# Kernel tuning notes

Hardware: AMD Instinct MI355X
Metric: run time of the kernel (lower is better)

Reference implementation:

```python
import jax, jax.numpy as jnp
import numpy as np

K = 3
KK = K * K


def _conv1x1(x, w, b):
    # x: [B,Ci,H,W], w: [Co,Ci]
    return jnp.einsum('bihw,oi->bohw', x, w) + b[None, :, None, None]


def _conv3x3(x, w, b):
    y = jax.lax.conv_general_dilated(x, w, (1, 1), ((1, 1), (1, 1)),
                                     dimension_numbers=('NCHW', 'OIHW', 'NCHW'))
    return y + b[None, :, None, None]


def _deform_conv3x3(x, offset, w, b):
    # Deformable conv v1, kernel 3x3, stride 1, pad 1, dilation 1, 1 deformable group.
    # x: [B,C,H,W]; offset: [B,2*KK,H,W] (dy,dx interleaved per kernel tap); w: [Co,C,3,3]
    B, C, H, W = x.shape
    dt = x.dtype
    off = offset.reshape(B, KK, 2, H, W)
    ky, kx = jnp.meshgrid(jnp.arange(K, dtype=dt), jnp.arange(K, dtype=dt), indexing='ij')
    ky = ky.reshape(KK)
    kx = kx.reshape(KK)
    # sampling locations: out_pos - pad + kernel_tap + learned offset
    base_y = jnp.arange(H, dtype=dt) - 1.0  # pad = 1
    base_x = jnp.arange(W, dtype=dt) - 1.0
    sy = base_y[None, None, :, None] + ky[None, :, None, None] + off[:, :, 0]  # [B,KK,H,W]
    sx = base_x[None, None, None, :] + kx[None, :, None, None] + off[:, :, 1]
    y0 = jnp.floor(sy)
    x0 = jnp.floor(sx)
    ty = sy - y0
    tx = sx - x0

    def gather(iy, ix):
        valid = ((iy >= 0) & (iy <= H - 1) & (ix >= 0) & (ix <= W - 1)).astype(dt)
        iyc = jnp.clip(iy, 0, H - 1).astype(jnp.int32)
        ixc = jnp.clip(ix, 0, W - 1).astype(jnp.int32)
        vals = jax.vmap(lambda img, a, c: img[:, a, c])(x, iyc, ixc)  # [B,C,KK,H,W]
        return vals * valid[:, None]

    w00 = ((1 - ty) * (1 - tx))[:, None]
    w01 = ((1 - ty) * tx)[:, None]
    w10 = (ty * (1 - tx))[:, None]
    w11 = (ty * tx)[:, None]
    sampled = (gather(y0, x0) * w00 + gather(y0, x0 + 1) * w01 +
               gather(y0 + 1, x0) * w10 + gather(y0 + 1, x0 + 1) * w11)  # [B,C,KK,H,W]
    Co = w.shape[0]
    out = jnp.einsum('bikhw,oik->bohw', sampled, w.reshape(Co, C, KK))
    return out + b[None, :, None, None]


def _branch(features, dw, db, ow, ob, tw, tb):
    h = _conv1x1(features, dw, db)
    off = _conv3x3(h, ow, ob)  # offset-predicting conv inside DFConv2d
    return jax.nn.relu(_deform_conv3x3(h, off, tw, tb))


def setup_inputs() -> dict:
    key = jax.random.key(0)
    ks = jax.random.split(key, 13)
    C = 256
    s1 = 1.0 / np.sqrt(C)          # kaiming_normal a=1 for 1x1 conv
    s3 = 1.0 / np.sqrt(C * KK)     # 3x3 conv
    so = 0.01                       # small offset-conv weights -> modest offsets
    f = lambda k, s, sc: jax.random.normal(k, s, dtype=jnp.float32) * sc
    return {
        'features': f(ks[0], (4, C, 64, 64), 1.0),
        'agg_down_w': f(ks[1], (C, C), s1),
        'agg_down_b': jnp.zeros((C,), jnp.float32),
        'agg_off_w': f(ks[2], (2 * KK, C, K, K), so),
        'agg_off_b': jnp.zeros((2 * KK,), jnp.float32),
        'agg_w': f(ks[3], (C, C, K, K), s3),
        'agg_b': jnp.zeros((C,), jnp.float32),
        'appr_down_w': f(ks[4], (C, C), s1),
        'appr_down_b': jnp.zeros((C,), jnp.float32),
        'appr_off_w': f(ks[5], (2 * KK, C, K, K), so),
        'appr_off_b': jnp.zeros((2 * KK,), jnp.float32),
        'appr_w': f(ks[6], (C, C, K, K), s3),
        'appr_b': jnp.zeros((C,), jnp.float32),
    }


def reference(features, agg_down_w, agg_down_b, agg_off_w, agg_off_b, agg_w, agg_b,
              appr_down_w, appr_down_b, appr_off_w, appr_off_b, appr_w, appr_b):
    agg = _branch(features, agg_down_w, agg_down_b, agg_off_w, agg_off_b, agg_w, agg_b)
    appr = _branch(features, appr_down_w, appr_down_b, appr_off_w, appr_off_b, appr_w, appr_b)
    return (agg, appr)
```

## Files before the change

### kernel.cpp

```cpp
#include <hip/hip_runtime.h>

#define HWP 4096
#define NPIX 4194304
#define KDIM 2304

typedef __attribute__((ext_vector_type(4))) float f32x4;
typedef __attribute__((ext_vector_type(4))) int   i32x4;
typedef __attribute__((ext_vector_type(8))) short short8;
typedef __attribute__((ext_vector_type(4))) unsigned short bf16x4;
typedef __attribute__((ext_vector_type(4))) unsigned short u16x4;

__device__ __forceinline__ unsigned short bf16_rne(float f) {
    unsigned int u = __builtin_bit_cast(unsigned int, f);
    u += 0x7FFFu + ((u >> 16) & 1u);
    return (unsigned short)(u >> 16);
}

__device__ __forceinline__ float bf2f(unsigned short u) {
    return __builtin_bit_cast(float, (unsigned int)u << 16);
}

__device__ __forceinline__ float u2f_lo(unsigned int u) {
    return __builtin_bit_cast(float, u << 16);
}

__device__ __forceinline__ float u2f_hi(unsigned int u) {
    return __builtin_bit_cast(float, u & 0xFFFF0000u);
}

__device__ __forceinline__ unsigned int cvt_pk_bf16(float lo, float hi) {
    unsigned int r;
    asm("v_cvt_pk_bf16_f32 %0, %1, %2" : "=v"(r) : "v"(lo), "v"(hi));
    return r;
}

__device__ __forceinline__ void gload_lds16(const void* g, void* l) {
    __builtin_amdgcn_global_load_lds((const __attribute__((address_space(1))) void*)g,
                                     (__attribute__((address_space(3))) void*)l, 16, 0, 0);
}

__global__ void prep_all_kernel(const float* __restrict__ x, unsigned short* __restrict__ fbt,
                                const float* __restrict__ dw0, const float* __restrict__ dw1,
                                const float* __restrict__ tw0, const float* __restrict__ tw1,
                                const float* __restrict__ ow0, const float* __restrict__ ow1,
                                unsigned short* __restrict__ w1b2,
                                unsigned short* __restrict__ w2A,
                                unsigned short* __restrict__ w2o) {
    __shared__ float T[64][65];
    int b = blockIdx.x;
    int t = threadIdx.x;
    if (b < 1024) {
        int pt = b & 63, ct = (b >> 6) & 3, bb = b >> 8;
        int lane = t & 63;
        int r = t >> 6;
        int c0 = ct * 64, p0 = pt * 64;
        const float* xb = x + (size_t)(bb * 256 + c0) * HWP + p0;
#pragma unroll
        for (int rr = 0; rr < 16; ++rr) {
            int ci = r * 16 + rr;
            T[ci][lane] = xb[(size_t)ci * HWP + lane];
        }
        __syncthreads();
        unsigned short* ob = fbt + ((size_t)bb * HWP + p0) * 256 + c0;
#pragma unroll
        for (int rr = 0; rr < 16; ++rr) {
            int px = r * 16 + rr;
            ob[(size_t)px * 256 + lane] = bf16_rne(T[lane][px]);
        }
        return;
    }
    int idx = (b - 1024) * 256 + t;
    if (idx < 131072) {
        int br = idx >> 16;
        int i  = idx & 65535;
        const float* dw = br ? dw1 : dw0;
        w1b2[idx] = bf16_rne(dw[i]);
    } else if (idx < 131072 + 1179648) {
        int j = idx - 131072;
        int br = j >= 589824;
        int i  = br ? j - 589824 : j;
        const float* tw = br ? tw1 : tw0;
        int cg = i / 147456;
        int r  = i - cg * 147456;
        int tap = r >> 14;
        int r2 = r & 16383;
        int s  = r2 >> 11;
        int fr = (r2 >> 9) & 3;
        int l  = (r2 >> 3) & 63;
        int e  = r2 & 7;
        int o  = cg * 64 + fr * 16 + (l & 15);
        int ci = s * 32 + ((l >> 4) << 3) + e;
        w2A[j] = bf16_rne(tw[(o * 256 + ci) * 9 + tap]);
    } else {
        int j = idx - 131072 - 1179648;
        int br = j >= 73728;
        int i  = br ? j - 73728 : j;
        const float* ow = br ? ow1 : ow0;
        int m = i / 2304;
        int k = i - m * 2304;
        int tap = k >> 8;
        int ci  = k & 255;
        w2o[j] = (m < 18) ? bf16_rne(ow[(m * 256 + ci) * 9 + tap]) : (unsigned short)0;
    }
}

__global__ void prep_w2_kernel(const float* __restrict__ tw0, const float* __restrict__ tw1,
                               unsigned short* __restrict__ w2) {
    int idx = blockIdx.x * 256 + threadIdx.x;
    int br = idx >= 589824;
    int i  = br ? idx - 589824 : idx;
    const float* tw = br ? tw1 : tw0;
    int ci = i & 255;
    int r  = i >> 8;
    int tap = r % 9;
    int o   = r / 9;
    w2[idx] = bf16_rne(tw[(o * 256 + ci) * 9 + tap]);
}

__global__ void prep_ow2_kernel(const float* __restrict__ ow0, const float* __restrict__ ow1,
                                float* __restrict__ owt) {
    int idx = blockIdx.x * 256 + threadIdx.x;
    int br = idx >= 41472;
    int i  = br ? idx - 41472 : idx;
    const float* ow = br ? ow1 : ow0;
    int co = i % 18;
    int r  = i / 18;
    int k  = r % 9;
    int ci = r / 9;
    owt[idx] = ow[(co * 256 + ci) * 9 + k];
}

__global__ void prep_w12_kernel(const float* __restrict__ dw0, const float* __restrict__ dw1,
                                unsigned short* __restrict__ w1b) {
    int idx = blockIdx.x * 256 + threadIdx.x;
    int br = idx >> 16;
    int i  = idx & 65535;
    const float* dw = br ? dw1 : dw0;
    w1b[idx] = bf16_rne(dw[i]);
}

__global__ void prep_fb16_kernel(const float* __restrict__ x, unsigned short* __restrict__ fbt) {
    __shared__ float T[64][65];
    int pt = blockIdx.x;
    int ct = blockIdx.y;
    int bb = blockIdx.z;
    int t = threadIdx.x;
    int lane = t & 63;
    int r = t >> 6;
    int c0 = ct * 64, p0 = pt * 64;
    const float* xb = x + (size_t)(bb * 256 + c0) * HWP + p0;
#pragma unroll
    for (int rr = 0; rr < 16; ++rr) {
        int ci = r * 16 + rr;
        T[ci][lane] = xb[(size_t)ci * HWP + lane];
    }
    __syncthreads();
    unsigned short* ob = fbt + ((size_t)bb * HWP + p0) * 256 + c0;
#pragma unroll
    for (int rr = 0; rr < 16; ++rr) {
        int px = r * 16 + rr;
        ob[(size_t)px * 256 + lane] = bf16_rne(T[lane][px]);
    }
}

__launch_bounds__(256)
__global__ void gemm1x1_kernel(const unsigned short* __restrict__ w1b2,
                               const unsigned short* __restrict__ fbt,
                               const float* __restrict__ db0, const float* __restrict__ db1,
                               float* __restrict__ h2, unsigned short* __restrict__ ht2,
                               int write_h) {
    __shared__ unsigned short As[128 * 64];
    __shared__ unsigned short Bs[64 * 64];
    int pt = blockIdx.x;
    int ot = blockIdx.y;
    int z  = blockIdx.z;
    int bb = z & 3;
    int br = z >> 2;
    const unsigned short* w1b = w1b2 + (size_t)br * 65536;
    const float* db = br ? db1 : db0;
    int t  = threadIdx.x;
    int l  = t & 63;
    int w  = t >> 6;
    int wr = w >> 1, wc = w & 1;
    int o0 = ot * 128, p0 = pt * 64;
    const unsigned short* fb = fbt + (size_t)bb * HWP * 256;
    f32x4 acc[4][2];
#pragma unroll
    for (int i = 0; i < 4; ++i)
#pragma unroll
        for (int j = 0; j < 2; ++j) acc[i][j] = (f32x4){0.f, 0.f, 0.f, 0.f};

    for (int ks = 0; ks < 4; ++ks) {
        int k0 = ks * 64;
#pragma unroll
        for (int rA = 0; rA < 4; ++rA) {
            int s = rA * 256 + t;
            int row = s >> 3, cg = (s & 7) ^ (row & 7);
            gload_lds16(w1b + (size_t)(o0 + row) * 256 + k0 + cg * 8, As + s * 8);
        }
#pragma unroll
        for (int rB = 0; rB < 2; ++rB) {
            int s = rB * 256 + t;
            int row = s >> 3, cg = (s & 7) ^ (row & 7);
            gload_lds16(fb + (size_t)(p0 + row) * 256 + k0 + cg * 8, Bs + s * 8);
        }
        __syncthreads();
#pragma unroll
        for (int half = 0; half < 2; ++half) {
            short8 a[4], b[2];
#pragma unroll
            for (int fr = 0; fr < 4; ++fr) {
                int row = wr * 64 + fr * 16 + (l & 15);
                int oct = half * 4 + (l >> 4);
                a[fr] = *reinterpret_cast<const short8*>(As + row * 64 + ((oct ^ (row & 7)) * 8));
            }
#pragma unroll
            for (int fc = 0; fc < 2; ++fc) {
                int row = wc * 32 + fc * 16 + (l & 15);
                int oct = half * 4 + (l >> 4);
                b[fc] = *reinterpret_cast<const short8*>(Bs + row * 64 + ((oct ^ (row & 7)) * 8));
            }
#pragma unroll
            for (int fr = 0; fr < 4; ++fr)
#pragma unroll
                for (int fc = 0; fc < 2; ++fc)
                    acc[fr][fc] = __builtin_amdgcn_mfma_f32_16x16x32_bf16(a[fr], b[fc], acc[fr][fc], 0, 0, 0);
        }
        __syncthreads();
    }

    float* hb = h2 + (size_t)br * NPIX + (size_t)bb * 256 * HWP;
    unsigned short* htb = ht2 + (size_t)br * NPIX + (size_t)bb * HWP * 256;
#pragma unroll
    for (int fr = 0; fr < 4; ++fr) {
        int o = o0 + wr * 64 + fr * 16 + ((l >> 4) << 2);
#pragma unroll
        for (int fc = 0; fc < 2; ++fc) {
            int p = p0 + wc * 32 + fc * 16 + (l & 15);
            f32x4 v;
#pragma unroll
            for (int reg = 0; reg < 4; ++reg) {
                v[reg] = acc[fr][fc][reg] + db[o + reg];
                if (write_h) hb[(size_t)(o + reg) * HWP + p] = v[reg];
            }
            uint2 pk;
            pk.x = cvt_pk_bf16(v[0], v[1]);
            pk.y = cvt_pk_bf16(v[2], v[3]);
            *reinterpret_cast<uint2*>(htb + (size_t)p * 256 + o) = pk;
        }
    }
}

__launch_bounds__(256)
__global__ void off_mfma_kernel(const unsigned short* __restrict__ w2o,
                                const unsigned short* __restrict__ ht2,
                                const float* __restrict__ ob0, const float* __restrict__ ob1,
                                float* __restrict__ dwq, unsigned short* __restrict__ dcq) {
    __shared__ float red[4][1152];
    int id = blockIdx.x;
    int br = id >> 8;
    int bb = (id >> 6) & 3;
    int y  = id & 63;
    const unsigned short* wA = w2o + (size_t)br * 73728;
    const unsigned short* htb = ht2 + (size_t)br * NPIX + (size_t)bb * HWP * 256;
    const float* ob = br ? ob1 : ob0;
    int t = threadIdx.x;
    int l = t & 63;
    int w = t >> 6;
    short8 zero = {};
    f32x4 acc[2][4];
#pragma unroll
    for (int i = 0; i < 2; ++i)
#pragma unroll
        for (int j = 0; j < 4; ++j) acc[i][j] = (f32x4){0.f, 0.f, 0.f, 0.f};

    for (int tap = 0; tap < 9; ++tap) {
        int ky = tap / 3, kx = tap % 3;
        int yy = y + ky - 1;
        bool vy = (yy >= 0) && (yy < 64);
        int cyy = min(max(yy, 0), 63);
#pragma unroll
        for (int sh = 0; sh < 2; ++sh) {
            int s = w * 2 + sh;
            short8 a[2], b[4];
#pragma unroll
            for (int fr = 0; fr < 2; ++fr)
                a[fr] = *reinterpret_cast<const short8*>(
                    wA + (size_t)(fr * 16 + (l & 15)) * KDIM + tap * 256 + s * 32 + ((l >> 4) << 3));
#pragma unroll
            for (int fc = 0; fc < 4; ++fc) {
                int px = fc * 16 + (l & 15);
                int xx = px + kx - 1;
                bool v = vy && (xx >= 0) && (xx < 64);
                int cxx = min(max(xx, 0), 63);
                short8 bv = *reinterpret_cast<const short8*>(
                    htb + (size_t)(cyy * 64 + cxx) * 256 + s * 32 + ((l >> 4) << 3));
                b[fc] = v ? bv : zero;
            }
#pragma unroll
            for (int fr = 0; fr < 2; ++fr)
#pragma unroll
                for (int fc = 0; fc < 4; ++fc)
                    acc[fr][fc] = __builtin_amdgcn_mfma_f32_16x16x32_bf16(a[fr], b[fc], acc[fr][fc], 0, 0, 0);
        }
    }

#pragma unroll
    for (int fr = 0; fr < 2; ++fr)
#pragma unroll
        for (int fc = 0; fc < 4; ++fc) {
            int px = fc * 16 + (l & 15);
#pragma unroll
            for (int reg = 0; reg < 4; ++reg) {
                int co = fr * 16 + ((l >> 4) << 2) + reg;
                if (co < 18) red[w][co * 64 + px] = acc[fr][fc][reg];
            }
        }
    __syncthreads();

    size_t dbase = ((size_t)(br * 4 + bb) * 9) * 4096 + (size_t)(y * 64);
    for (int e = t; e < 576; e += 256) {
        int tap = e >> 6, px = e & 63;
        int c0 = 2 * tap, c1 = 2 * tap + 1;
        float dy = ob[c0] + red[0][c0 * 64 + px] + red[1][c0 * 64 + px]
                          + red[2][c0 * 64 + px] + red[3][c0 * 64 + px];
        float dx = ob[c1] + red[0][c1 * 64 + px] + red[1][c1 * 64 + px]
                          + red[2][c1 * 64 + px] + red[3][c1 * 64 + px];
        int ky = tap / 3, kx = tap % 3;
        float sy = (float)(y - 1 + ky) + dy;
        float sx = (float)(px - 1 + kx) + dx;
        float y0f = floorf(sy), x0f = floorf(sx);
        float ty = sy - y0f, tx = sx - x0f;
        int iy0 = (int)y0f, ix0 = (int)x0f;
        int iy1 = iy0 + 1, ix1 = ix0 + 1;
        bool vy0 = (iy0 >= 0) & (iy0 < 64);
        bool vy1 = (iy1 >= 0) & (iy1 < 64);
        bool vx0 = (ix0 >= 0) & (ix0 < 64);
        bool vx1 = (ix1 >= 0) & (ix1 < 64);
        int cy0 = min(max(iy0, 0), 63), cy1 = min(max(iy1, 0), 63);
        int cx0 = min(max(ix0, 0), 63), cx1 = min(max(ix1, 0), 63);
        f32x4 ww;
        ww[0] = (1.f - ty) * (1.f - tx) * ((vy0 & vx0) ? 1.f : 0.f);
        ww[1] = (1.f - ty) * tx * ((vy0 & vx1) ? 1.f : 0.f);
        ww[2] = ty * (1.f - tx) * ((vy1 & vx0) ? 1.f : 0.f);
        ww[3] = ty * tx * ((vy1 & vx1) ? 1.f : 0.f);
        u16x4 pc;
        pc[0] = (unsigned short)(cy0 * 64 + cx0);
        pc[1] = (unsigned short)(cy0 * 64 + cx1);
        pc[2] = (unsigned short)(cy1 * 64 + cx0);
        pc[3] = (unsigned short)(cy1 * 64 + cx1);
        size_t di = dbase + (size_t)tap * 4096 + px;
        *reinterpret_cast<f32x4*>(dwq + di * 4) = ww;
        *reinterpret_cast<u16x4*>(dcq + di * 4) = pc;
    }
}

__global__ void off_conv_part_kernel(const float* __restrict__ h2, const float* __restrict__ owt2,
                                     float* __restrict__ part2) {
    int y  = blockIdx.x & 63;
    int bb = blockIdx.x >> 6;
    int c  = blockIdx.y;
    int br = blockIdx.z;
    const float* h = h2 + (size_t)br * NPIX;
    const float* owt = owt2 + (size_t)br * 41472;
    float* part = part2 + (size_t)br * 2359296;
    int t  = threadIdx.x;
    int x  = t & 63;
    int wv = __builtin_amdgcn_readfirstlane(t >> 6);
    int  toff[9];
    bool tval[9];
#pragma unroll
    for (int ky = 0; ky < 3; ++ky) {
        int yy = y + ky - 1;
        bool vy = (yy >= 0) && (yy < 64);
        int cyy = min(max(yy, 0), 63);
#pragma unroll
        for (int kx = 0; kx < 3; ++kx) {
            int xx = x + kx - 1;
            tval[ky * 3 + kx] = vy && (xx >= 0) && (xx < 64);
            toff[ky * 3 + kx] = cyy * 64 + min(max(xx, 0), 63);
        }
    }
    float acc[18];
#pragma unroll
    for (int co = 0; co < 18; ++co) acc[co] = 0.f;
    int ci0 = c * 32 + wv * 8;
    const float* hb = h + (size_t)(bb * 256 + ci0) * HWP;
#pragma unroll
    for (int i = 0; i < 8; ++i) {
        const float* hc = hb + i * HWP;
        const float* wci = owt + (size_t)(ci0 + i) * 162;
#pragma unroll
        for (int k = 0; k < 9; ++k) {
            float hv = hc[toff[k]];
            hv = tval[k] ? hv : 0.f;
            const float* wk = wci + k * 18;
#pragma unroll
            for (int co = 0; co < 18; ++co)
                acc[co] = fmaf(wk[co], hv, acc[co]);
        }
    }
    __shared__ float red[4][18][64];
    int wvl = t >> 6;
#pragma unroll
    for (int co = 0; co < 18; ++co) red[wvl][co][x] = acc[co];
    __syncthreads();
    if (wvl == 0) {
#pragma unroll
        for (int co = 0; co < 18; ++co) {
            float s = red[0][co][x] + red[1][co][x] + red[2][co][x] + red[3][co][x];
            part[(size_t)c * 294912 + ((bb * 18 + co) << 12) + (y << 6) + x] = s;
        }
    }
}

__global__ void off_reduce2_kernel(const float* __restrict__ part2,
                                   const float* __restrict__ ob0, const float* __restrict__ ob1,
                                   float* __restrict__ off2) {
    int idx = blockIdx.x * 256 + threadIdx.x;
    int br = idx >= 294912;
    int i  = br ? idx - 294912 : idx;
    const float* part = part2 + (size_t)br * 2359296;
    const float* b = br ? ob1 : ob0;
    int co = (i >> 12) % 18;
    float s = b[co];
#pragma unroll
    for (int c = 0; c < 8; ++c) s += part[(size_t)c * 294912 + i];
    off2[idx] = s;
}

__launch_bounds__(256, 2)
__global__ void dgemm_fused_kernel(const unsigned short* __restrict__ w2b,
                                   const unsigned short* __restrict__ ht2,
                                   const float* __restrict__ dwq,
                                   const unsigned short* __restrict__ dcq,
                                   const float* __restrict__ tb0,
                                   const float* __restrict__ tb1,
                                   float* __restrict__ out) {
    __shared__ unsigned short Bs[2][64 * 256];
    int id = blockIdx.x;
    int sw = (id & 7) * 64 + (id >> 3);
    int br = sw >> 8;
    int mt = sw & 255;
    int bb = mt >> 6;
    int y  = mt & 63;
    const unsigned short* w2f = w2b + (size_t)br * 589824;
    const unsigned short* htb = ht2 + (size_t)br * NPIX + (size_t)bb * HWP * 256;
    const float* bias = br ? tb1 : tb0;
    size_t dbase = ((size_t)(br * 4 + bb) * 9) * 4096 + (size_t)(y * 64);
    int t = threadIdx.x;
    int l = t & 63;
    int w = t >> 6;
    int wvu = __builtin_amdgcn_readfirstlane(w);
    int le = l << 2;

    f32x4 acc[4][4];
#pragma unroll
    for (int i = 0; i < 4; ++i)
#pragma unroll
        for (int j = 0; j < 4; ++j) acc[i][j] = (f32x4){0.f, 0.f, 0.f, 0.f};

#define STAGE_B(TAPV, WB)                                                          \
    do {                                                                           \
        const float* dwt = dwq + (dbase + (size_t)(TAPV) * 4096) * 4;              \
        const unsigned short* dct = dcq + (dbase + (size_t)(TAPV) * 4096) * 4;     \
        _Pragma("unroll")                                                          \
        for (int i_ = 0; i_ < 16; ++i_) {                                          \
            int px = wvu * 16 + i_;                                                \
            f32x4 ww = *reinterpret_cast<const f32x4*>(dwt + (size_t)px * 4);      \
            u16x4 pc = *reinterpret_cast<const u16x4*>(dct + (size_t)px * 4);      \
            int b00 = ((int)pc[0] << 8) + le;                                      \
            int b01 = ((int)pc[1] << 8) + le;                                      \
            int b10 = ((int)pc[2] << 8) + le;                                      \
            int b11 = ((int)pc[3] << 8) + le;                                      \
            uint2 u00 = *reinterpret_cast<const uint2*>(htb + b00);                \
            uint2 u01 = *reinterpret_cast<const uint2*>(htb + b01);                \
            uint2 u10 = *reinterpret_cast<const uint2*>(htb + b10);                \
            uint2 u11 = *reinterpret_cast<const uint2*>(htb + b11);                \
            float s0 = fmaf(ww[0], u2f_lo(u00.x),                                  \
                       fmaf(ww[1], u2f_lo(u01.x),                                  \
                       fmaf(ww[2], u2f_lo(u10.x), ww[3] * u2f_lo(u11.x))));        \
            float s1 = fmaf(ww[0], u2f_hi(u00.x),                                  \
                       fmaf(ww[1], u2f_hi(u01.x),                                  \
                       fmaf(ww[2], u2f_hi(u10.x), ww[3] * u2f_hi(u11.x))));        \
            float s2 = fmaf(ww[0], u2f_lo(u00.y),                                  \
                       fmaf(ww[1], u2f_lo(u01.y),                                  \
                       fmaf(ww[2], u2f_lo(u10.y), ww[3] * u2f_lo(u11.y))));        \
            float s3 = fmaf(ww[0], u2f_hi(u00.y),                                  \
                       fmaf(ww[1], u2f_hi(u01.y),                                  \
                       fmaf(ww[2], u2f_hi(u10.y), ww[3] * u2f_hi(u11.y))));        \
            uint2 pk;                                                              \
            pk.x = cvt_pk_bf16(s0, s1);                                            \
            pk.y = cvt_pk_bf16(s2, s3);                                            \
            int g = l >> 1, sub = l & 1;                                           \
            *reinterpret_cast<uint2*>((WB) + px * 256 +                            \
                (((g ^ (px & 7)) << 3) | (sub << 2))) = pk;                        \
        }                                                                          \
    } while (0)

#define COMPUTE_TAP(TAPV, RB)                                                      \
    do {                                                                           \
        const unsigned short* wtapf = w2f + (size_t)(wvu * 9 + (TAPV)) * 16384;    \
        short8 aA[4], aB[4];                                                       \
        _Pragma("unroll")                                                          \
        for (int fr = 0; fr < 4; ++fr)                                             \
            aA[fr] = *reinterpret_cast<const short8*>(wtapf + fr * 512 + (l << 3));\
        _Pragma("unroll")                                                          \
        for (int fr = 0; fr < 4; ++fr)                                             \
            aB[fr] = *reinterpret_cast<const short8*>(wtapf + (4 + fr) * 512 + (l << 3)); \
        _Pragma("unroll")                                                          \
        for (int s = 0; s < 8; ++s) {                                              \
            short8 aC[4];                                                          \
            if (s < 6) {                                                           \
                _Pragma("unroll")                                                  \
                for (int fr = 0; fr < 4; ++fr)                                     \
                    aC[fr] = *reinterpret_cast<const short8*>(                     \
                        wtapf + (size_t)((s + 2) * 4 + fr) * 512 + (l << 3));      \
            }                                                                      \
            short8 b[4];                                                           \
            _Pragma("unroll")                                                      \
            for (int fc = 0; fc < 4; ++fc) {                                       \
                int prow = fc * 16 + (l & 15);                                     \
                int cg8 = (s << 2) + (l >> 4);                                     \
                b[fc] = *reinterpret_cast<const short8*>(                          \
                    (RB) + prow * 256 + ((cg8 ^ (prow & 7)) << 3));                \
            }                                                                      \
            __builtin_amdgcn_s_setprio(1);                                         \
            _Pragma("unroll")                                                      \
            for (int fr = 0; fr < 4; ++fr)                                         \
                _Pragma("unroll")                                                  \
                for (int fc = 0; fc < 4; ++fc)                                     \
                    acc[fr][fc] = __builtin_amdgcn_mfma_f32_16x16x32_bf16(         \
                        aA[fr], b[fc], acc[fr][fc], 0, 0, 0);                      \
            __builtin_amdgcn_s_setprio(0);                                         \
            if (s < 7) {                                                           \
                _Pragma("unroll")                                                  \
                for (int fr = 0; fr < 4; ++fr) { aA[fr] = aB[fr]; aB[fr] = aC[fr]; } \
            }                                                                      \
        }                                                                          \
    } while (0)

    STAGE_B(0, Bs[0]);
    __syncthreads();
#pragma unroll 1
    for (int it = 0; it < 4; ++it) {
        int tap = it * 2;
        COMPUTE_TAP(tap, Bs[0]);
        STAGE_B(tap + 1, Bs[1]);
        __syncthreads();
        COMPUTE_TAP(tap + 1, Bs[1]);
        STAGE_B(tap + 2, Bs[0]);
        __syncthreads();
    }
    COMPUTE_TAP(8, Bs[0]);
#undef STAGE_B
#undef COMPUTE_TAP

    float* outp = out + (size_t)br * NPIX + (size_t)(bb * 256) * HWP + y * 64;
#pragma unroll
    for (int fr = 0; fr < 4; ++fr) {
        int o = wvu * 64 + fr * 16 + ((l >> 4) << 2);
#pragma unroll
        for (int fc = 0; fc < 4; ++fc) {
            int pxc = fc * 16 + (l & 15);
#pragma unroll
            for (int reg = 0; reg < 4; ++reg) {
                float v = acc[fr][fc][reg] + bias[o + reg];
                outp[(size_t)(o + reg) * HWP + pxc] = fmaxf(v, 0.f);
            }
        }
    }
}

__launch_bounds__(256)
__global__ void sample2_kernel(const unsigned short* __restrict__ ht, const float* __restrict__ off,
                               unsigned short* __restrict__ sm, int b0) {
    int y   = blockIdx.x;
    int tap = blockIdx.y;
    int bb  = b0 + blockIdx.z;
    int t   = threadIdx.x;
    int lane = t & 63;
    int wv  = t >> 6;
    int ky = tap / 3, kx = tap % 3;
    const unsigned short* htb = ht + (size_t)bb * HWP * 256;
    const float* offy = off + ((bb * 18 + 2 * tap) * 64 + y) * 64;
    const float* offx = off + ((bb * 18 + 2 * tap + 1) * 64 + y) * 64;
    int mrow = ((bb - b0) * 64 + y) * 64;
#pragma unroll 4
    for (int i = 0; i < 16; ++i) {
        int px = wv * 16 + i;
        float dy = offy[px];
        float dx = offx[px];
        float sy = (float)(y - 1 + ky) + dy;
        float sx = (float)(px - 1 + kx) + dx;
        float y0f = floorf(sy), x0f = floorf(sx);
        float ty = sy - y0f, tx = sx - x0f;
        int iy0 = (int)y0f, ix0 = (int)x0f;
        int iy1 = iy0 + 1, ix1 = ix0 + 1;
        bool vy0 = (iy0 >= 0) & (iy0 < 64);
        bool vy1 = (iy1 >= 0) & (iy1 < 64);
        bool vx0 = (ix0 >= 0) & (ix0 < 64);
        bool vx1 = (ix1 >= 0) & (ix1 < 64);
        int cy0 = min(max(iy0, 0), 63), cy1 = min(max(iy1, 0), 63);
        int cx0 = min(max(ix0, 0), 63), cx1 = min(max(ix1, 0), 63);
        float w00 = (1.f - ty) * (1.f - tx) * ((vy0 & vx0) ? 1.f : 0.f);
        float w01 = (1.f - ty) * tx * ((vy0 & vx1) ? 1.f : 0.f);
        float w10 = ty * (1.f - tx) * ((vy1 & vx0) ? 1.f : 0.f);
        float w11 = ty * tx * ((vy1 & vx1) ? 1.f : 0.f);
        int le = lane << 2;
        bf16x4 q00 = *reinterpret_cast<const bf16x4*>(htb + ((cy0 * 64 + cx0) << 8) + le);
        bf16x4 q01 = *reinterpret_cast<const bf16x4*>(htb + ((cy0 * 64 + cx1) << 8) + le);
        bf16x4 q10 = *reinterpret_cast<const bf16x4*>(htb + ((cy1 * 64 + cx0) << 8) + le);
        bf16x4 q11 = *reinterpret_cast<const bf16x4*>(htb + ((cy1 * 64 + cx1) << 8) + le);
        f32x4 s;
#pragma unroll
        for (int j = 0; j < 4; ++j)
            s[j] = fmaf(w00, bf2f(q00[j]),
                   fmaf(w01, bf2f(q01[j]),
                   fmaf(w10, bf2f(q10[j]), w11 * bf2f(q11[j]))));
        uint2 pk;
        pk.x = cvt_pk_bf16(s[0], s[1]);
        pk.y = cvt_pk_bf16(s[2], s[3]);
        *reinterpret_cast<uint2*>(sm + (size_t)(mrow + px) * KDIM + tap * 256 + lane * 4) = pk;
    }
}

__launch_bounds__(256)
__global__ void gemm2_kernel(const unsigned short* __restrict__ w2b,
                             const unsigned short* __restrict__ smb, size_t smstride,
                             const float* __restrict__ tb0, const float* __restrict__ tb1,
                             float* __restrict__ out, int mbase) {
    __shared__ unsigned short As[128 * 64];
    __shared__ unsigned short Bs[64 * 64];
    int mt = blockIdx.x;
    int ot = blockIdx.y;
    int br = blockIdx.z;
    const unsigned short* w2 = w2b + (size_t)br * 589824;
    const unsigned short* sm = smb + (size_t)br * smstride;
    const float* bias = br ? tb1 : tb0;
    float* outp = out + (size_t)br * NPIX;
    int t  = threadIdx.x;
    int l  = t & 63;
    int w  = t >> 6;
    int wr = w >> 1, wc = w & 1;
    int o0 = ot * 128, m0 = mt * 64;
    f32x4 acc[4][2];
#pragma unroll
    for (int i = 0; i < 4; ++i)
#pragma unroll
        for (int j = 0; j < 2; ++j) acc[i][j] = (f32x4){0.f, 0.f, 0.f, 0.f};

    for (int ks = 0; ks < KDIM / 64; ++ks) {
        int k0 = ks * 64;
#pragma unroll
        for (int rA = 0; rA < 4; ++rA) {
            int s = rA * 256 + t;
            int row = s >> 3, cg = (s & 7) ^ (row & 7);
            gload_lds16(w2 + (size_t)(o0 + row) * KDIM + k0 + cg * 8, As + s * 8);
        }
#pragma unroll
        for (int rB = 0; rB < 2; ++rB) {
            int s = rB * 256 + t;
            int row = s >> 3, cg = (s & 7) ^ (row & 7);
            gload_lds16(sm + (size_t)(m0 + row) * KDIM + k0 + cg * 8, Bs + s * 8);
        }
        __syncthreads();
#pragma unroll
        for (int half = 0; half < 2; ++half) {
            short8 a[4], b[2];
#pragma unroll
            for (int fr = 0; fr < 4; ++fr) {
                int row = wr * 64 + fr * 16 + (l & 15);
                int oct = half * 4 + (l >> 4);
                a[fr] = *reinterpret_cast<const short8*>(As + row * 64 + ((oct ^ (row & 7)) * 8));
            }
#pragma unroll
            for (int fc = 0; fc < 2; ++fc) {
                int row = wc * 32 + fc * 16 + (l & 15);
                int oct = half * 4 + (l >> 4);
                b[fc] = *reinterpret_cast<const short8*>(Bs + row * 64 + ((oct ^ (row & 7)) * 8));
            }
#pragma unroll
            for (int fr = 0; fr < 4; ++fr)
#pragma unroll
                for (int fc = 0; fc < 2; ++fc)
                    acc[fr][fc] = __builtin_amdgcn_mfma_f32_16x16x32_bf16(a[fr], b[fc], acc[fr][fc], 0, 0, 0);
        }
        __syncthreads();
    }

#pragma unroll
    for (int fr = 0; fr < 4; ++fr) {
        int o = o0 + wr * 64 + fr * 16 + ((l >> 4) << 2);
#pragma unroll
        for (int fc = 0; fc < 2; ++fc) {
            int mg = mbase + m0 + wc * 32 + fc * 16 + (l & 15);
            int bbv = mg >> 12;
            int pix = mg & 4095;
            float* op = outp + (size_t)(bbv * 256) * HWP + pix;
#pragma unroll
            for (int reg = 0; reg < 4; ++reg) {
                float v = acc[fr][fc][reg] + bias[o + reg];
                op[(size_t)(o + reg) * HWP] = fmaxf(v, 0.f);
            }
        }
    }
}

extern "C" void kernel_launch(void* const* d_in, const int* in_sizes, int n_in,
                              void* d_out, int out_size, void* d_ws, size_t ws_size,
                              hipStream_t stream) {
    const float* feat = (const float*)d_in[0];
    char* base = (char*)d_ws;
    float* outp = (float*)d_out;
    const size_t perb = (size_t)HWP * KDIM * 2;

    const float* dw0 = (const float*)d_in[1];
    const float* db0 = (const float*)d_in[2];
    const float* ow0 = (const float*)d_in[3];
    const float* ob0 = (const float*)d_in[4];
    const float* tw0 = (const float*)d_in[5];
    const float* tb0 = (const float*)d_in[6];
    const float* dw1 = (const float*)d_in[7];
    const float* db1 = (const float*)d_in[8];
    const float* ow1 = (const float*)d_in[9];
    const float* ob1 = (const float*)d_in[10];
    const float* tw1 = (const float*)d_in[11];
    const float* tb1 = (const float*)d_in[12];

    bool tierA = ws_size >= 47218688;

    if (tierA) {
        unsigned short* ht2 = (unsigned short*)base;
        unsigned short* w2A = (unsigned short*)(base + 35913728);
        unsigned short* w2o = (unsigned short*)(base + 38273024);
        unsigned short* fbt = (unsigned short*)(base + 38567936);
        unsigned short* w1b2 = (unsigned short*)(base + 46956544);
        float* dwq = (float*)(base + 38567936);
        unsigned short* dcq = (unsigned short*)(base + 38567936 + 4718592);

        hipLaunchKernelGGL(prep_all_kernel, dim3(6720), dim3(256), 0, stream,
                           feat, fbt, dw0, dw1, tw0, tw1, ow0, ow1, w1b2, w2A, w2o);
        hipLaunchKernelGGL(gemm1x1_kernel, dim3(64, 2, 8), dim3(256), 0, stream,
                           w1b2, fbt, db0, db1, (float*)nullptr, ht2, 0);
        hipLaunchKernelGGL(off_mfma_kernel, dim3(512), dim3(256), 0, stream,
                           w2o, ht2, ob0, ob1, dwq, dcq);
        hipLaunchKernelGGL(dgemm_fused_kernel, dim3(512), dim3(256), 0, stream,
                           w2A, ht2, dwq, dcq, tb0, tb1, outp);
        return;
    }

    float* h   = (float*)base;
    float* off = h + NPIX;
    unsigned short* w2 = (unsigned short*)(base + 17956864);
    float* owt = (float*)(base + 19136512);
    unsigned short* ht = (unsigned short*)(base + 19302400);
    unsigned short* smN = (unsigned short*)(base + 27691008);
    float* partN = (float*)(base + 27691008);
    unsigned short* fbtN = (unsigned short*)(base + 27691008 + 9437184);
    unsigned short* w1bN = (unsigned short*)(base + 27691008 + 17825792);

    int nb = 0;
    if (27691008 + 4 * perb <= ws_size) nb = 4;
    else if (27691008 + 2 * perb <= ws_size) nb = 2;
    else nb = 1;

    for (int br = 0; br < 2; ++br) {
        const float* dw = (const float*)d_in[1 + 6 * br];
        const float* db = (const float*)d_in[2 + 6 * br];
        const float* ow = (const float*)d_in[3 + 6 * br];
        const float* ob = (const float*)d_in[4 + 6 * br];
        const float* tw = (const float*)d_in[5 + 6 * br];
        const float* tb = (const float*)d_in[6 + 6 * br];

        hipLaunchKernelGGL(prep_fb16_kernel, dim3(64, 4, 4), dim3(256), 0, stream, feat, fbtN);
        hipLaunchKernelGGL(prep_w12_kernel, dim3(256), dim3(256), 0, stream, dw, dw, w1bN);
        hipLaunchKernelGGL(gemm1x1_kernel, dim3(64, 2, 4), dim3(256), 0, stream,
                           w1bN, fbtN, db, db, h, ht, 1);
        hipLaunchKernelGGL(prep_ow2_kernel, dim3(162), dim3(256), 0, stream, ow, ow, owt);
        hipLaunchKernelGGL(off_conv_part_kernel, dim3(256, 8, 1), dim3(256), 0, stream,
                           h, owt, partN);
        hipLaunchKernelGGL(off_reduce2_kernel, dim3(1152), dim3(256), 0, stream,
                           partN, ob, ob, off);
        hipLaunchKernelGGL(prep_w2_kernel, dim3(2304), dim3(256), 0, stream, tw, tw, w2);

        for (int b0 = 0; b0 < 4; b0 += nb) {
            hipLaunchKernelGGL(sample2_kernel, dim3(64, 9, nb), dim3(256), 0, stream,
                               ht, off, smN, b0);
            hipLaunchKernelGGL(gemm2_kernel, dim3(nb * 64, 2, 1), dim3(256), 0, stream,
                               w2, smN, (size_t)0, tb, tb, outp + br * NPIX, b0 * HWP);
        }
    }
}
```

Measured before the change: 122.1 us.

## Interleave deformable sampling gather with MFMA compute inside each tap

The bilinear gather and LDS staging for the next tap is now split into per-pixel pieces, two per k-step, and interleaved with the MFMA loop of the current tap instead of running as a separate phase. The aim is to hide global-load latency of the gather behind matrix math. The A-fragment register rotation becomes a 3-slot ring buffer indexed by step, and the loop runs per tap with a computed buffer parity. This may raise register pressure and can disturb the instruction schedule.

Result: no change. 122.4 us (+0.3%).

```diff
diff --git a/kernel.cpp b/kernel.cpp
--- a/kernel.cpp
+++ b/kernel.cpp
@@ -460,62 +460,61 @@
 #pragma unroll
         for (int j = 0; j < 4; ++j) acc[i][j] = (f32x4){0.f, 0.f, 0.f, 0.f};
 
-#define STAGE_B(TAPV, WB)                                                          \
+#define STAGE_PX(PX, WB)                                                           \
     do {                                                                           \
-        const float* dwt = dwq + (dbase + (size_t)(TAPV) * 4096) * 4;              \
-        const unsigned short* dct = dcq + (dbase + (size_t)(TAPV) * 4096) * 4;     \
-        _Pragma("unroll")                                                          \
-        for (int i_ = 0; i_ < 16; ++i_) {                                          \
-            int px = wvu * 16 + i_;                                                \
-            f32x4 ww = *reinterpret_cast<const f32x4*>(dwt + (size_t)px * 4);      \
-            u16x4 pc = *reinterpret_cast<const u16x4*>(dct + (size_t)px * 4);      \
-            int b00 = ((int)pc[0] << 8) + le;                                      \
-            int b01 = ((int)pc[1] << 8) + le;                                      \
-            int b10 = ((int)pc[2] << 8) + le;                                      \
-            int b11 = ((int)pc[3] << 8) + le;                                      \
-            uint2 u00 = *reinterpret_cast<const uint2*>(htb + b00);                \
-            uint2 u01 = *reinterpret_cast<const uint2*>(htb + b01);                \
-            uint2 u10 = *reinterpret_cast<const uint2*>(htb + b10);                \
-            uint2 u11 = *reinterpret_cast<const uint2*>(htb + b11);                \
-            float s0 = fmaf(ww[0], u2f_lo(u00.x),                                  \
-                       fmaf(ww[1], u2f_lo(u01.x),                                  \
-                       fmaf(ww[2], u2f_lo(u10.x), ww[3] * u2f_lo(u11.x))));        \
-            float s1 = fmaf(ww[0], u2f_hi(u00.x),                                  \
-                       fmaf(ww[1], u2f_hi(u01.x),                                  \
-                       fmaf(ww[2], u2f_hi(u10.x), ww[3] * u2f_hi(u11.x))));        \
-            float s2 = fmaf(ww[0], u2f_lo(u00.y),                                  \
-                       fmaf(ww[1], u2f_lo(u01.y),                                  \
-                       fmaf(ww[2], u2f_lo(u10.y), ww[3] * u2f_lo(u11.y))));        \
-            float s3 = fmaf(ww[0], u2f_hi(u00.y),                                  \
-                       fmaf(ww[1], u2f_hi(u01.y),                                  \
-                       fmaf(ww[2], u2f_hi(u10.y), ww[3] * u2f_hi(u11.y))));        \
-            uint2 pk;                                                              \
-            pk.x = cvt_pk_bf16(s0, s1);                                            \
-            pk.y = cvt_pk_bf16(s2, s3);                                            \
-            int g = l >> 1, sub = l & 1;                                           \
-            *reinterpret_cast<uint2*>((WB) + px * 256 +                            \
-                (((g ^ (px & 7)) << 3) | (sub << 2))) = pk;                        \
-        }                                                                          \
+        int px_ = (PX);                                                            \
+        f32x4 ww = *reinterpret_cast<const f32x4*>(dwt + (size_t)px_ * 4);         \
+        u16x4 pc = *reinterpret_cast<const u16x4*>(dct + (size_t)px_ * 4);         \
+        int b00 = ((int)pc[0] << 8) + le;                                          \
+        int b01 = ((int)pc[1] << 8) + le;                                          \
+        int b10 = ((int)pc[2] << 8) + le;                                          \
+        int b11 = ((int)pc[3] << 8) + le;                                          \
+        uint2 u00 = *reinterpret_cast<const uint2*>(htb + b00);                    \
+        uint2 u01 = *reinterpret_cast<const uint2*>(htb + b01);                    \
+        uint2 u10 = *reinterpret_cast<const uint2*>(htb + b10);                    \
+        uint2 u11 = *reinterpret_cast<const uint2*>(htb + b11);                    \
+        float s0 = fmaf(ww[0], u2f_lo(u00.x),                                      \
+                   fmaf(ww[1], u2f_lo(u01.x),                                      \
+                   fmaf(ww[2], u2f_lo(u10.x), ww[3] * u2f_lo(u11.x))));            \
+        float s1 = fmaf(ww[0], u2f_hi(u00.x),                                      \
+                   fmaf(ww[1], u2f_hi(u01.x),                                      \
+                   fmaf(ww[2], u2f_hi(u10.x), ww[3] * u2f_hi(u11.x))));            \
+        float s2 = fmaf(ww[0], u2f_lo(u00.y),                                      \
+                   fmaf(ww[1], u2f_lo(u01.y),                                      \
+                   fmaf(ww[2], u2f_lo(u10.y), ww[3] * u2f_lo(u11.y))));            \
+        float s3 = fmaf(ww[0], u2f_hi(u00.y),                                      \
+                   fmaf(ww[1], u2f_hi(u01.y),                                      \
+                   fmaf(ww[2], u2f_hi(u10.y), ww[3] * u2f_hi(u11.y))));            \
+        uint2 pk;                                                                  \
+        pk.x = cvt_pk_bf16(s0, s1);                                                \
+        pk.y = cvt_pk_bf16(s2, s3);                                                \
+        int g = l >> 1, sub = l & 1;                                               \
+        *reinterpret_cast<uint2*>((WB) + px_ * 256 +                               \
+            (((g ^ (px_ & 7)) << 3) | (sub << 2))) = pk;                           \
     } while (0)
 
-#define COMPUTE_TAP(TAPV, RB)                                                      \
+#define TAP_BODY(TAPV, RB, WB, DO_STAGE)                                           \
     do {                                                                           \
         const unsigned short* wtapf = w2f + (size_t)(wvu * 9 + (TAPV)) * 16384;    \
-        short8 aA[4], aB[4];                                                       \
+        const float* dwt = dwq + (dbase + (size_t)((TAPV) + 1) * 4096) * 4;        \
+        const unsigned short* dct = dcq + (dbase + (size_t)((TAPV) + 1) * 4096) * 4; \
+        short8 areg[3][4];                                                         \
         _Pragma("unroll")                                                          \
-        for (int fr = 0; fr < 4; ++fr)                                             \
-            aA[fr] = *reinterpret_cast<const short8*>(wtapf + fr * 512 + (l << 3));\
-        _Pragma("unroll")                                                          \
-        for (int fr = 0; fr < 4; ++fr)                                             \
-            aB[fr] = *reinterpret_cast<const short8*>(wtapf + (4 + fr) * 512 + (l << 3)); \
+        for (int fr = 0; fr < 4; ++fr) {                                           \
+            areg[0][fr] = *reinterpret_cast<const short8*>(wtapf + fr * 512 + (l << 3)); \
+            areg[1][fr] = *reinterpret_cast<const short8*>(wtapf + (4 + fr) * 512 + (l << 3)); \
+        }                                                                          \
         _Pragma("unroll")                                                          \
         for (int s = 0; s < 8; ++s) {                                              \
-            short8 aC[4];                                                          \
             if (s < 6) {                                                           \
                 _Pragma("unroll")                                                  \
                 for (int fr = 0; fr < 4; ++fr)                                     \
-                    aC[fr] = *reinterpret_cast<const short8*>(                     \
+                    areg[(s + 2) % 3][fr] = *reinterpret_cast<const short8*>(      \
                         wtapf + (size_t)((s + 2) * 4 + fr) * 512 + (l << 3));      \
+            }                                                                      \
+            if (DO_STAGE) {                                                        \
+                STAGE_PX(wvu * 16 + s * 2 + 0, WB);                                \
+                STAGE_PX(wvu * 16 + s * 2 + 1, WB);                                \
             }                                                                      \
             short8 b[4];                                                           \
             _Pragma("unroll")                                                      \
@@ -531,30 +530,30 @@
                 _Pragma("unroll")                                                  \
                 for (int fc = 0; fc < 4; ++fc)                                     \
                     acc[fr][fc] = __builtin_amdgcn_mfma_f32_16x16x32_bf16(         \
-                        aA[fr], b[fc], acc[fr][fc], 0, 0, 0);                      \
+                        areg[s % 3][fr], b[fc], acc[fr][fc], 0, 0, 0);             \
             __builtin_amdgcn_s_setprio(0);                                         \
-            if (s < 7) {                                                           \
-                _Pragma("unroll")                                                  \
-                for (int fr = 0; fr < 4; ++fr) { aA[fr] = aB[fr]; aB[fr] = aC[fr]; } \
-            }                                                                      \
         }                                                                          \
     } while (0)
 
-    STAGE_B(0, Bs[0]);
+    {
+        const float* dwt = dwq + (dbase + (size_t)0 * 4096) * 4;
+        const unsigned short* dct = dcq + (dbase + (size_t)0 * 4096) * 4;
+#pragma unroll
+        for (int i_ = 0; i_ < 16; ++i_) {
+            STAGE_PX(wvu * 16 + i_, Bs[0]);
+        }
+    }
     __syncthreads();
 #pragma unroll 1
-    for (int it = 0; it < 4; ++it) {
-        int tap = it * 2;
-        COMPUTE_TAP(tap, Bs[0]);
-        STAGE_B(tap + 1, Bs[1]);
+    for (int tap = 0; tap < 8; ++tap) {
+        unsigned short* rb = Bs[tap & 1];
+        unsigned short* wb = Bs[(tap + 1) & 1];
+        TAP_BODY(tap, rb, wb, 1);
         __syncthreads();
-        COMPUTE_TAP(tap + 1, Bs[1]);
-        STAGE_B(tap + 2, Bs[0]);
-        __syncthreads();
-    }
-    COMPUTE_TAP(8, Bs[0]);
-#undef STAGE_B
-#undef COMPUTE_TAP
+    }
+    TAP_BODY(8, Bs[0], Bs[1], 0);
+#undef TAP_BODY
+#undef STAGE_PX
 
     float* outp = out + (size_t)br * NPIX + (size_t)(bb * 256) * HWP + y * 64;
 #pragma unroll
```

## Warp-specialize deformable GEMM into producer gather and consumer MFMA waves

Applied to the files above, without the earlier changes.

Doubles the block to 512 threads and splits the waves by role: four waves gather and bilinearly interpolate the next tap's samples into LDS while the other four run MFMA on the current tap, synchronising once per tap instead of alternating stage and compute in the same waves. The producer batches its weight and index loads before the gathers, and the consumer rotates three A-fragment register buffers by index instead of copying them. This aims to overlap gather latency with matrix math, at the cost of higher per-block resource use that may reduce occupancy and leaves half the waves idle in each phase.

Measured after the change: 124.3 us. No clear change (+1.8%).

```diff
diff --git a/kernel.cpp b/kernel.cpp
--- a/kernel.cpp
+++ b/kernel.cpp
@@ -429,7 +429,7 @@
     off2[idx] = s;
 }
 
-__launch_bounds__(256, 2)
+__launch_bounds__(512, 2)
 __global__ void dgemm_fused_kernel(const unsigned short* __restrict__ w2b,
                                    const unsigned short* __restrict__ ht2,
                                    const float* __restrict__ dwq,
@@ -452,6 +452,8 @@
     int l = t & 63;
     int w = t >> 6;
     int wvu = __builtin_amdgcn_readfirstlane(w);
+    int pw  = wvu & 3;
+    bool isCons = (wvu < 4);
     int le = l << 2;
 
     f32x4 acc[4][4];
@@ -460,61 +462,65 @@
 #pragma unroll
         for (int j = 0; j < 4; ++j) acc[i][j] = (f32x4){0.f, 0.f, 0.f, 0.f};
 
-#define STAGE_B(TAPV, WB)                                                          \
+#define STAGE_TAP(TAPV, WB)                                                        \
     do {                                                                           \
         const float* dwt = dwq + (dbase + (size_t)(TAPV) * 4096) * 4;              \
         const unsigned short* dct = dcq + (dbase + (size_t)(TAPV) * 4096) * 4;     \
+        f32x4 dwv[16];                                                             \
+        u16x4 dcv[16];                                                             \
         _Pragma("unroll")                                                          \
         for (int i_ = 0; i_ < 16; ++i_) {                                          \
-            int px = wvu * 16 + i_;                                                \
-            f32x4 ww = *reinterpret_cast<const f32x4*>(dwt + (size_t)px * 4);      \
-            u16x4 pc = *reinterpret_cast<const u16x4*>(dct + (size_t)px * 4);      \
-            int b00 = ((int)pc[0] << 8) + le;                                      \
-            int b01 = ((int)pc[1] << 8) + le;                                      \
-            int b10 = ((int)pc[2] << 8) + le;                                      \
-            int b11 = ((int)pc[3] << 8) + le;                                      \
+            int px_ = pw * 16 + i_;                                                \
+            dwv[i_] = *reinterpret_cast<const f32x4*>(dwt + (size_t)px_ * 4);      \
+            dcv[i_] = *reinterpret_cast<const u16x4*>(dct + (size_t)px_ * 4);      \
+        }                                                                          \
+        _Pragma("unroll")                                                          \
+        for (int i_ = 0; i_ < 16; ++i_) {                                          \
+            int px_ = pw * 16 + i_;                                                \
+            int b00 = ((int)dcv[i_][0] << 8) + le;                                 \
+            int b01 = ((int)dcv[i_][1] << 8) + le;                                 \
+            int b10 = ((int)dcv[i_][2] << 8) + le;                                 \
+            int b11 = ((int)dcv[i_][3] << 8) + le;                                 \
             uint2 u00 = *reinterpret_cast<const uint2*>(htb + b00);                \
             uint2 u01 = *reinterpret_cast<const uint2*>(htb + b01);                \
             uint2 u10 = *reinterpret_cast<const uint2*>(htb + b10);                \
             uint2 u11 = *reinterpret_cast<const uint2*>(htb + b11);                \
-            float s0 = fmaf(ww[0], u2f_lo(u00.x),                                  \
-                       fmaf(ww[1], u2f_lo(u01.x),                                  \
-                       fmaf(ww[2], u2f_lo(u10.x), ww[3] * u2f_lo(u11.x))));        \
-            float s1 = fmaf(ww[0], u2f_hi(u00.x),                                  \
-                       fmaf(ww[1], u2f_hi(u01.x),                                  \
-                       fmaf(ww[2], u2f_hi(u10.x), ww[3] * u2f_hi(u11.x))));        \
-            float s2 = fmaf(ww[0], u2f_lo(u00.y),                                  \
-                       fmaf(ww[1], u2f_lo(u01.y),                                  \
-                       fmaf(ww[2], u2f_lo(u10.y), ww[3] * u2f_lo(u11.y))));        \
-            float s3 = fmaf(ww[0], u2f_hi(u00.y),                                  \
-                       fmaf(ww[1], u2f_hi(u01.y),                                  \
-                       fmaf(ww[2], u2f_hi(u10.y), ww[3] * u2f_hi(u11.y))));        \
+            float s0 = fmaf(dwv[i_][0], u2f_lo(u00.x),                             \
+                       fmaf(dwv[i_][1], u2f_lo(u01.x),                             \
+                       fmaf(dwv[i_][2], u2f_lo(u10.x), dwv[i_][3] * u2f_lo(u11.x)))); \
+            float s1 = fmaf(dwv[i_][0], u2f_hi(u00.x),                             \
+                       fmaf(dwv[i_][1], u2f_hi(u01.x),                             \
+                       fmaf(dwv[i_][2], u2f_hi(u10.x), dwv[i_][3] * u2f_hi(u11.x)))); \
+            float s2 = fmaf(dwv[i_][0], u2f_lo(u00.y),                             \
+                       fmaf(dwv[i_][1], u2f_lo(u01.y),                             \
+                       fmaf(dwv[i_][2], u2f_lo(u10.y), dwv[i_][3] * u2f_lo(u11.y)))); \
+            float s3 = fmaf(dwv[i_][0], u2f_hi(u00.y),                             \
+                       fmaf(dwv[i_][1], u2f_hi(u01.y),                             \
+                       fmaf(dwv[i_][2], u2f_hi(u10.y), dwv[i_][3] * u2f_hi(u11.y)))); \
             uint2 pk;                                                              \
             pk.x = cvt_pk_bf16(s0, s1);                                            \
             pk.y = cvt_pk_bf16(s2, s3);                                            \
             int g = l >> 1, sub = l & 1;                                           \
-            *reinterpret_cast<uint2*>((WB) + px * 256 +                            \
-                (((g ^ (px & 7)) << 3) | (sub << 2))) = pk;                        \
+            *reinterpret_cast<uint2*>((WB) + px_ * 256 +                           \
+                (((g ^ (px_ & 7)) << 3) | (sub << 2))) = pk;                       \
         }                                                                          \
     } while (0)
 
 #define COMPUTE_TAP(TAPV, RB)                                                      \
     do {                                                                           \
-        const unsigned short* wtapf = w2f + (size_t)(wvu * 9 + (TAPV)) * 16384;    \
-        short8 aA[4], aB[4];                                                       \
+        const unsigned short* wtapf = w2f + (size_t)(pw * 9 + (TAPV)) * 16384;     \
+        short8 areg[3][4];                                                         \
         _Pragma("unroll")                                                          \
-        for (int fr = 0; fr < 4; ++fr)                                             \
-            aA[fr] = *reinterpret_cast<const short8*>(wtapf + fr * 512 + (l << 3));\
-        _Pragma("unroll")                                                          \
-        for (int fr = 0; fr < 4; ++fr)                                             \
-            aB[fr] = *reinterpret_cast<const short8*>(wtapf + (4 + fr) * 512 + (l << 3)); \
+        for (int fr = 0; fr < 4; ++fr) {                                           \
+            areg[0][fr] = *reinterpret_cast<const short8*>(wtapf + fr * 512 + (l << 3)); \
+            areg[1][fr] = *reinterpret_cast<const short8*>(wtapf + (4 + fr) * 512 + (l << 3)); \
+        }                                                                          \
         _Pragma("unroll")                                                          \
         for (int s = 0; s < 8; ++s) {                                              \
-            short8 aC[4];                                                          \
             if (s < 6) {                                                           \
                 _Pragma("unroll")                                                  \
                 for (int fr = 0; fr < 4; ++fr)                                     \
-                    aC[fr] = *reinterpret_cast<const short8*>(                     \
+                    areg[(s + 2) % 3][fr] = *reinterpret_cast<const short8*>(      \
                         wtapf + (size_t)((s + 2) * 4 + fr) * 512 + (l << 3));      \
             }                                                                      \
             short8 b[4];                                                           \
@@ -531,45 +537,41 @@
                 _Pragma("unroll")                                                  \
                 for (int fc = 0; fc < 4; ++fc)                                     \
                     acc[fr][fc] = __builtin_amdgcn_mfma_f32_16x16x32_bf16(         \
-                        aA[fr], b[fc], acc[fr][fc], 0, 0, 0);                      \
+                        areg[s % 3][fr], b[fc], acc[fr][fc], 0, 0, 0);             \
             __builtin_amdgcn_s_setprio(0);                                         \
-            if (s < 7) {                                                           \
-                _Pragma("unroll")                                                  \
-                for (int fr = 0; fr < 4; ++fr) { aA[fr] = aB[fr]; aB[fr] = aC[fr]; } \
-            }                                                                      \
         }                                                                          \
     } while (0)
 
-    STAGE_B(0, Bs[0]);
+    if (!isCons) STAGE_TAP(0, Bs[0]);
     __syncthreads();
 #pragma unroll 1
-    for (int it = 0; it < 4; ++it) {
-        int tap = it * 2;
-        COMPUTE_TAP(tap, Bs[0]);
-        STAGE_B(tap + 1, Bs[1]);
+    for (int tap = 0; tap < 8; ++tap) {
+        if (isCons) {
+            COMPUTE_TAP(tap, Bs[tap & 1]);
+        } else {
+            STAGE_TAP(tap + 1, Bs[(tap + 1) & 1]);
+        }
         __syncthreads();
-        COMPUTE_TAP(tap + 1, Bs[1]);
-        STAGE_B(tap + 2, Bs[0]);
-        __syncthreads();
-    }
-    COMPUTE_TAP(8, Bs[0]);
-#undef STAGE_B
+    }
+    if (isCons) {
+        COMPUTE_TAP(8, Bs[0]);
+        float* outp = out + (size_t)br * NPIX + (size_t)(bb * 256) * HWP + y * 64;
+#pragma unroll
+        for (int fr = 0; fr < 4; ++fr) {
+            int o = pw * 64 + fr * 16 + ((l >> 4) << 2);
+#pragma unroll
+            for (int fc = 0; fc < 4; ++fc) {
+                int pxc = fc * 16 + (l & 15);
+#pragma unroll
+                for (int reg = 0; reg < 4; ++reg) {
+                    float v = acc[fr][fc][reg] + bias[o + reg];
+                    outp[(size_t)(o + reg) * HWP + pxc] = fmaxf(v, 0.f);
+                }
+            }
+        }
+    }
+#undef STAGE_TAP
 #undef COMPUTE_TAP
-
-    float* outp = out + (size_t)br * NPIX + (size_t)(bb * 256) * HWP + y * 64;
-#pragma unroll
-    for (int fr = 0; fr < 4; ++fr) {
-        int o = wvu * 64 + fr * 16 + ((l >> 4) << 2);
-#pragma unroll
-        for (int fc = 0; fc < 4; ++fc) {
-            int pxc = fc * 16 + (l & 15);
-#pragma unroll
-            for (int reg = 0; reg < 4; ++reg) {
-                float v = acc[fr][fc][reg] + bias[o + reg];
-                outp[(size_t)(o + reg) * HWP + pxc] = fmaxf(v, 0.f);
-            }
-        }
-    }
 }
 
 __launch_bounds__(256)
@@ -745,7 +747,7 @@
                            w1b2, fbt, db0, db1, (float*)nullptr, ht2, 0);
         hipLaunchKernelGGL(off_mfma_kernel, dim3(512), dim3(256), 0, stream,
                            w2o, ht2, ob0, ob1, dwq, dcq);
-        hipLaunchKernelGGL(dgemm_fused_kernel, dim3(512), dim3(256), 0, stream,
+        hipLaunchKernelGGL(dgemm_fused_kernel, dim3(512), dim3(512), 0, stream,
                            w2A, ht2, dwq, dcq, tb0, tb1, outp);
         return;
     }
```

## Halve dgemm pixel tile to 32 and raise occupancy to four blocks per CU

Applied to the files above, without the earlier changes.

The fused deformable GEMM kernel now processes 32 pixels per block instead of 64, doubling the grid to 1024 blocks and halving LDS and accumulator usage so launch bounds can request four blocks per CU. A-operand prefetch is reduced from a three-stage to a two-stage register ring, and the tap loop is restructured to stage the next tap before computing the current one, with a single barrier per tap. This aims to improve latency hiding through occupancy and better overlap of gather and MFMA. The cost is that each weight fragment is reused over half as many pixels, so weight traffic from global or cache doubles.

New measurement: 128.7 us. 1.05x slower.

```diff
diff --git a/kernel.cpp b/kernel.cpp
--- a/kernel.cpp
+++ b/kernel.cpp
@@ -429,7 +429,7 @@
     off2[idx] = s;
 }
 
-__launch_bounds__(256, 2)
+__launch_bounds__(256, 4)
 __global__ void dgemm_fused_kernel(const unsigned short* __restrict__ w2b,
                                    const unsigned short* __restrict__ ht2,
                                    const float* __restrict__ dwq,
@@ -437,38 +437,38 @@
                                    const float* __restrict__ tb0,
                                    const float* __restrict__ tb1,
                                    float* __restrict__ out) {
-    __shared__ unsigned short Bs[2][64 * 256];
+    __shared__ unsigned short Bs[2][32 * 256];
     int id = blockIdx.x;
-    int sw = (id & 7) * 64 + (id >> 3);
-    int br = sw >> 8;
-    int mt = sw & 255;
-    int bb = mt >> 6;
-    int y  = mt & 63;
+    int sw = (id & 7) * 128 + (id >> 3);
+    int br = sw >> 9;
+    int bb = (sw >> 7) & 3;
+    int y  = (sw >> 1) & 63;
+    int half = sw & 1;
     const unsigned short* w2f = w2b + (size_t)br * 589824;
     const unsigned short* htb = ht2 + (size_t)br * NPIX + (size_t)bb * HWP * 256;
     const float* bias = br ? tb1 : tb0;
-    size_t dbase = ((size_t)(br * 4 + bb) * 9) * 4096 + (size_t)(y * 64);
+    size_t dbase = ((size_t)(br * 4 + bb) * 9) * 4096 + (size_t)(y * 64 + half * 32);
     int t = threadIdx.x;
     int l = t & 63;
     int w = t >> 6;
-    int wvu = __builtin_amdgcn_readfirstlane(w);
+    int pw = __builtin_amdgcn_readfirstlane(w);
     int le = l << 2;
 
-    f32x4 acc[4][4];
+    f32x4 acc[4][2];
 #pragma unroll
     for (int i = 0; i < 4; ++i)
 #pragma unroll
-        for (int j = 0; j < 4; ++j) acc[i][j] = (f32x4){0.f, 0.f, 0.f, 0.f};
-
-#define STAGE_B(TAPV, WB)                                                          \
+        for (int j = 0; j < 2; ++j) acc[i][j] = (f32x4){0.f, 0.f, 0.f, 0.f};
+
+#define STAGE_TAP(TAPV, WB)                                                        \
     do {                                                                           \
         const float* dwt = dwq + (dbase + (size_t)(TAPV) * 4096) * 4;              \
         const unsigned short* dct = dcq + (dbase + (size_t)(TAPV) * 4096) * 4;     \
         _Pragma("unroll")                                                          \
-        for (int i_ = 0; i_ < 16; ++i_) {                                          \
-            int px = wvu * 16 + i_;                                                \
-            f32x4 ww = *reinterpret_cast<const f32x4*>(dwt + (size_t)px * 4);      \
-            u16x4 pc = *reinterpret_cast<const u16x4*>(dct + (size_t)px * 4);      \
+        for (int i_ = 0; i_ < 8; ++i_) {                                           \
+            int px_ = pw * 8 + i_;                                                 \
+            f32x4 ww = *reinterpret_cast<const f32x4*>(dwt + (size_t)px_ * 4);     \
+            u16x4 pc = *reinterpret_cast<const u16x4*>(dct + (size_t)px_ * 4);     \
             int b00 = ((int)pc[0] << 8) + le;                                      \
             int b01 = ((int)pc[1] << 8) + le;                                      \
             int b10 = ((int)pc[2] << 8) + le;                                      \
@@ -493,33 +493,29 @@
             pk.x = cvt_pk_bf16(s0, s1);                                            \
             pk.y = cvt_pk_bf16(s2, s3);                                            \
             int g = l >> 1, sub = l & 1;                                           \
-            *reinterpret_cast<uint2*>((WB) + px * 256 +                            \
-                (((g ^ (px & 7)) << 3) | (sub << 2))) = pk;                        \
+            *reinterpret_cast<uint2*>((WB) + px_ * 256 +                           \
+                (((g ^ (px_ & 7)) << 3) | (sub << 2))) = pk;                       \
         }                                                                          \
     } while (0)
 
 #define COMPUTE_TAP(TAPV, RB)                                                      \
     do {                                                                           \
-        const unsigned short* wtapf = w2f + (size_t)(wvu * 9 + (TAPV)) * 16384;    \
-        short8 aA[4], aB[4];                                                       \
+        const unsigned short* wtapf = w2f + (size_t)(pw * 9 + (TAPV)) * 16384;     \
+        short8 areg[2][4];                                                         \
         _Pragma("unroll")                                                          \
         for (int fr = 0; fr < 4; ++fr)                                             \
-            aA[fr] = *reinterpret_cast<const short8*>(wtapf + fr * 512 + (l << 3));\
-        _Pragma("unroll")                                                          \
-        for (int fr = 0; fr < 4; ++fr)                                             \
-            aB[fr] = *reinterpret_cast<const short8*>(wtapf + (4 + fr) * 512 + (l << 3)); \
+            areg[0][fr] = *reinterpret_cast<const short8*>(wtapf + fr * 512 + (l << 3)); \
         _Pragma("unroll")                                                          \
         for (int s = 0; s < 8; ++s) {                                              \
-            short8 aC[4];                                                          \
-            if (s < 6) {                                                           \
+            if (s < 7) {                                                           \
                 _Pragma("unroll")                                                  \
                 for (int fr = 0; fr < 4; ++fr)                                     \
-                    aC[fr] = *reinterpret_cast<const short8*>(                     \
-                        wtapf + (size_t)((s + 2) * 4 + fr) * 512 + (l << 3));      \
+                    areg[(s + 1) & 1][fr] = *reinterpret_cast<const short8*>(      \
+                        wtapf + (size_t)((s + 1) * 4 + fr) * 512 + (l << 3));      \
             }                                                                      \
-            short8 b[4];                                                           \
+            short8 b[2];                                                           \
             _Pragma("unroll")                                                      \
-            for (int fc = 0; fc < 4; ++fc) {                                       \
+            for (int fc = 0; fc < 2; ++fc) {                                       \
                 int prow = fc * 16 + (l & 15);                                     \
                 int cg8 = (s << 2) + (l >> 4);                                     \
                 b[fc] = *reinterpret_cast<const short8*>(                          \
@@ -529,39 +525,31 @@
             _Pragma("unroll")                                                      \
             for (int fr = 0; fr < 4; ++fr)                                         \
                 _Pragma("unroll")                                                  \
-                for (int fc = 0; fc < 4; ++fc)                                     \
+                for (int fc = 0; fc < 2; ++fc)                                     \
                     acc[fr][fc] = __builtin_amdgcn_mfma_f32_16x16x32_bf16(         \
-                        aA[fr], b[fc], acc[fr][fc], 0, 0, 0);                      \
+                        areg[s & 1][fr], b[fc], acc[fr][fc], 0, 0, 0);             \
             __builtin_amdgcn_s_setprio(0);                                         \
-            if (s < 7) {                                                           \
-                _Pragma("unroll")                                                  \
-                for (int fr = 0; fr < 4; ++fr) { aA[fr] = aB[fr]; aB[fr] = aC[fr]; } \
-            }                                                                      \
         }                                                                          \
     } while (0)
 
-    STAGE_B(0, Bs[0]);
+    STAGE_TAP(0, Bs[0]);
     __syncthreads();
 #pragma unroll 1
-    for (int it = 0; it < 4; ++it) {
-        int tap = it * 2;
-        COMPUTE_TAP(tap, Bs[0]);
-        STAGE_B(tap + 1, Bs[1]);
+    for (int tap = 0; tap < 8; ++tap) {
+        STAGE_TAP(tap + 1, Bs[(tap + 1) & 1]);
+        COMPUTE_TAP(tap, Bs[tap & 1]);
         __syncthreads();
-        COMPUTE_TAP(tap + 1, Bs[1]);
-        STAGE_B(tap + 2, Bs[0]);
-        __syncthreads();
     }
     COMPUTE_TAP(8, Bs[0]);
-#undef STAGE_B
+#undef STAGE_TAP
 #undef COMPUTE_TAP
 
-    float* outp = out + (size_t)br * NPIX + (size_t)(bb * 256) * HWP + y * 64;
+    float* outp = out + (size_t)br * NPIX + (size_t)(bb * 256) * HWP + y * 64 + half * 32;
 #pragma unroll
     for (int fr = 0; fr < 4; ++fr) {
-        int o = wvu * 64 + fr * 16 + ((l >> 4) << 2);
-#pragma unroll
-        for (int fc = 0; fc < 4; ++fc) {
+        int o = pw * 64 + fr * 16 + ((l >> 4) << 2);
+#pragma unroll
+        for (int fc = 0; fc < 2; ++fc) {
             int pxc = fc * 16 + (l & 15);
 #pragma unroll
             for (int reg = 0; reg < 4; ++reg) {
@@ -745,7 +733,7 @@
                            w1b2, fbt, db0, db1, (float*)nullptr, ht2, 0);
         hipLaunchKernelGGL(off_mfma_kernel, dim3(512), dim3(256), 0, stream,
                            w2o, ht2, ob0, ob1, dwq, dcq);
-        hipLaunchKernelGGL(dgemm_fused_kernel, dim3(512), dim3(256), 0, stream,
+        hipLaunchKernelGGL(dgemm_fused_kernel, dim3(1024), dim3(256), 0, stream,
                            w2A, ht2, dwq, dcq, tb0, tb1, outp);
         return;
     }
```
